# Performance work log

Hardware: AMD Instinct MI355X
Metric: run time of the kernel (lower is better)

## Reference

```python
import jax, jax.numpy as jnp
import numpy as np

RADIUS = 0.2
K = 32  # num_neighbors


def ball_query(centers, points, radius, k):
    """centers [B,3,M], points [B,3,N] -> int32 indices [B,M,k].
    Matches PointNet++ CUDA semantics: first k points (in original order)
    with squared distance < radius^2; slots beyond the count are filled
    with the first valid index (0 if no point is in the ball)."""
    cn = jnp.sum(centers * centers, axis=1)              # [B,M]
    pn = jnp.sum(points * points, axis=1)                # [B,N]
    cross = jnp.einsum('bdm,bdn->bmn', centers, points)  # [B,M,N]
    d2 = cn[:, :, None] + pn[:, None, :] - 2.0 * cross   # [B,M,N]
    valid = d2 < radius * radius
    # stable argsort puts valid indices first, preserving original order
    order = jnp.argsort(jnp.logical_not(valid), axis=-1, stable=True)
    idx = order[..., :k]                                  # [B,M,k]
    count = jnp.sum(valid, axis=-1, keepdims=True)        # [B,M,1]
    fill = idx[..., :1]                                   # first valid (or 0)
    return jnp.where(jnp.arange(k)[None, None, :] < count, idx, fill)


def group(features, idx):
    """features [B,C,N], idx [B,M,K] -> [B,C,M,K]."""
    return jax.vmap(lambda f, i: jnp.take(f, i, axis=1))(features, idx)


def setup_inputs() -> dict:
    key = jax.random.key(0)
    k1, k2, k3, k4 = jax.random.split(key, 4)
    B, N, M, C, CT = 8, 8192, 2048, 64, 64
    return {
        'points_coords': jax.random.uniform(k1, (B, 3, N), dtype=jnp.float32),
        'centers_coords': jax.random.uniform(k2, (B, 3, M), dtype=jnp.float32),
        'temb': jax.random.normal(k3, (B, CT, N), dtype=jnp.float32),
        'points_features': jax.random.normal(k4, (B, C, N), dtype=jnp.float32),
    }


def reference(points_coords, centers_coords, temb, points_features):
    idx = ball_query(centers_coords, points_coords, RADIUS, K)           # [B,M,K]
    neighbor_coords = group(points_coords, idx) - centers_coords[:, :, :, None]  # [B,3,M,K]
    neighbor_features = jnp.concatenate(
        [neighbor_coords, group(points_features, idx)], axis=1)          # [B,3+C,M,K]
    temb_grouped = group(temb, idx)                                      # [B,CT,M,K]
    return neighbor_features, temb_grouped
```

## Files before the change

### kernel.cpp

```cpp
#include <hip/hip_runtime.h>

#define B  8
#define N  8192
#define M  2048
#define C  64
#define CT 64
#define K  32
#define R2 0.04f

__global__ __launch_bounds__(256) void transpose_kernel(
    const float* __restrict__ points,
    const float* __restrict__ temb,
    const float* __restrict__ feats,
    float* __restrict__ pointsT,
    float* __restrict__ tembT,
    float* __restrict__ featsT)
{
    const int gx = blockIdx.x;
    if (gx < 2048) {
        const int a  = gx >> 10;
        const int tt = gx & 1023;
        const int b  = tt >> 7;
        const int n0 = (tt & 127) << 6;
        const float* src = (a ? temb : feats) + (size_t)b * 64 * N;
        float* dst = (a ? tembT : featsT) + (size_t)b * N * 64;
        __shared__ float lds[64][65];
        const int nl = threadIdx.x & 63;
        const int c0 = threadIdx.x >> 6;
        #pragma unroll
        for (int i = 0; i < 16; ++i) {
            const int c = c0 + i * 4;
            lds[c][nl] = src[(size_t)c * N + n0 + nl];
        }
        __syncthreads();
        #pragma unroll
        for (int i = 0; i < 16; ++i) {
            const int n = c0 + i * 4;
            dst[(size_t)(n0 + n) * 64 + nl] = lds[nl][n];
        }
    } else {
        const int tt = gx - 2048;
        const int b  = tt >> 5;
        const int n  = ((tt & 31) << 8) + threadIdx.x;
        const float* pc = points + (size_t)b * 3 * N;
        float* dst = pointsT + ((size_t)b * N + n) * 4;
        dst[0] = pc[n];
        dst[1] = pc[N + n];
        dst[2] = pc[2 * N + n];
    }
}

__global__ __launch_bounds__(256) void ball_query_kernel(
    const float* __restrict__ points,
    const float* __restrict__ centers,
    int* __restrict__ idx)
{
    __shared__ int sidx[4][K];
    const int wave = threadIdx.x >> 6;
    const int lane = threadIdx.x & 63;
    const int center_id = blockIdx.x * 4 + wave;
    const int b = center_id / M;
    const int m = center_id - b * M;

    const float* pc = points + b * 3 * N;
    const float cx = centers[(b * 3 + 0) * M + m];
    const float cy = centers[(b * 3 + 1) * M + m];
    const float cz = centers[(b * 3 + 2) * M + m];
    const float cn = __fadd_rn(__fadd_rn(__fmul_rn(cx, cx), __fmul_rn(cy, cy)),
                               __fmul_rn(cz, cz));

    if (lane == 0) sidx[wave][0] = 0;

    int cnt = 0;
    for (int base = 0; base < N; base += 64) {
        const int n = base + lane;
        const float px = pc[n];
        const float py = pc[N + n];
        const float pz = pc[2 * N + n];
        const float pn = __fadd_rn(__fadd_rn(__fmul_rn(px, px), __fmul_rn(py, py)),
                                   __fmul_rn(pz, pz));
        const float cross = __fadd_rn(__fadd_rn(__fmul_rn(cx, px), __fmul_rn(cy, py)),
                                      __fmul_rn(cz, pz));
        const float d2 = __fsub_rn(__fadd_rn(cn, pn), __fmul_rn(2.0f, cross));
        const bool valid = d2 < R2;
        const unsigned long long mask = __ballot(valid);
        if (valid) {
            const int slot = cnt + __popcll(mask & ((1ull << lane) - 1ull));
            if (slot < K) sidx[wave][slot] = n;
        }
        cnt += (int)__popcll(mask);
        if (cnt >= K) break;
    }
    __syncthreads();

    if (lane < K) {
        const int fill = sidx[wave][0];
        const int v = sidx[wave][lane];
        idx[center_id * K + lane] = (lane < cnt) ? v : fill;
    }
}

__global__ __launch_bounds__(256) void gather_kernel(
    const float* __restrict__ pointsT,
    const float* __restrict__ centers,
    const float* __restrict__ tembT,
    const float* __restrict__ featsT,
    const int* __restrict__ idx,
    float* __restrict__ out1,
    float* __restrict__ out2)
{
    __shared__ int   sn[128];
    __shared__ float tile[128 * 65];
    __shared__ float ctile[3][128];

    const int t = threadIdx.x;
    const int MB4 = M / 4;
    const int b  = blockIdx.x / MB4;
    const int m0 = (blockIdx.x - b * MB4) * 4;
    const size_t base_mk = (size_t)m0 * K;
    const size_t cs = (size_t)M * K;

    if (t < 128) sn[t] = idx[((size_t)b * M + m0) * K + t];
    __syncthreads();

    const int cq = t & 15;
    const int pl = t >> 4;
    const float* fT = featsT + (size_t)b * N * 64;
    const float* tT = tembT  + (size_t)b * N * 64;

    #pragma unroll
    for (int i = 0; i < 8; ++i) {
        const int p = i * 16 + pl;
        const int n = sn[p];
        const float4 v = *(const float4*)(fT + (size_t)n * 64 + cq * 4);
        float* d = &tile[p * 65 + cq * 4];
        d[0] = v.x; d[1] = v.y; d[2] = v.z; d[3] = v.w;
    }
    __syncthreads();
    {
        const int p   = t & 127;
        const int ch0 = t >> 7;
        float* o = out1 + (size_t)b * 67 * cs + 3 * cs + base_mk + p;
        #pragma unroll
        for (int i = 0; i < 32; ++i) {
            const int c = ch0 + i * 2;
            o[(size_t)c * cs] = tile[p * 65 + c];
        }
    }
    __syncthreads();

    #pragma unroll
    for (int i = 0; i < 8; ++i) {
        const int p = i * 16 + pl;
        const int n = sn[p];
        const float4 v = *(const float4*)(tT + (size_t)n * 64 + cq * 4);
        float* d = &tile[p * 65 + cq * 4];
        d[0] = v.x; d[1] = v.y; d[2] = v.z; d[3] = v.w;
    }
    __syncthreads();
    {
        const int p   = t & 127;
        const int ch0 = t >> 7;
        float* o = out2 + (size_t)b * 64 * cs + base_mk + p;
        #pragma unroll
        for (int i = 0; i < 32; ++i) {
            const int c = ch0 + i * 2;
            o[(size_t)c * cs] = tile[p * 65 + c];
        }
    }

    if (t < 128) {
        const int p = t;
        const int n = sn[p];
        const int m = m0 + (p >> 5);
        const float4 v = *(const float4*)(pointsT + ((size_t)b * N + n) * 4);
        ctile[0][p] = v.x - centers[((size_t)b * 3 + 0) * M + m];
        ctile[1][p] = v.y - centers[((size_t)b * 3 + 1) * M + m];
        ctile[2][p] = v.z - centers[((size_t)b * 3 + 2) * M + m];
    }
    __syncthreads();
    {
        const int c = t >> 7;
        const int p = t & 127;
        out1[((size_t)b * 67 + c) * cs + base_mk + p] = ctile[c][p];
    }
    if (t < 128) {
        out1[((size_t)b * 67 + 2) * cs + base_mk + t] = ctile[2][t];
    }
}

extern "C" void kernel_launch(void* const* d_in, const int* in_sizes, int n_in,
                              void* d_out, int out_size, void* d_ws, size_t ws_size,
                              hipStream_t stream) {
    const float* points  = (const float*)d_in[0];
    const float* centers = (const float*)d_in[1];
    const float* temb    = (const float*)d_in[2];
    const float* feats   = (const float*)d_in[3];

    int*   idx     = (int*)d_ws;
    float* pointsT = (float*)((char*)d_ws + (2u << 20));
    float* featsT  = pointsT + (size_t)B * N * 4;
    float* tembT   = featsT  + (size_t)B * N * 64;

    float* out1 = (float*)d_out;
    float* out2 = out1 + (size_t)B * (3 + C) * M * K;

    transpose_kernel<<<2304, 256, 0, stream>>>(points, temb, feats,
                                               pointsT, tembT, featsT);
    ball_query_kernel<<<(B * M) / 4, 256, 0, stream>>>(points, centers, idx);
    gather_kernel<<<(B * M) / 4, 256, 0, stream>>>(pointsT, centers, tembT,
                                                   featsT, idx, out1, out2);
}
```

Before: 382.3 us.

## Fuse ball query into gather kernel with prefetched float4 point loads

Merges the ball-query kernel into the gather kernel. Each wave now finds its center's neighbor indices straight into shared memory, so the idx buffer round trip and one launch go away. The search reads the transposed float4 point array in batches of 8, double-buffered, and uses mbcnt to rank lanes. The cost is more registers in the fused kernel, and the block's gather phase now waits on the slowest wave's search.

```diff
diff --git a/kernel.cpp b/kernel.cpp
--- a/kernel.cpp
+++ b/kernel.cpp
@@ -47,65 +47,37 @@
         dst[0] = pc[n];
         dst[1] = pc[N + n];
         dst[2] = pc[2 * N + n];
+        dst[3] = 0.0f;
     }
 }
 
-__global__ __launch_bounds__(256) void ball_query_kernel(
-    const float* __restrict__ points,
-    const float* __restrict__ centers,
-    int* __restrict__ idx)
-{
-    __shared__ int sidx[4][K];
-    const int wave = threadIdx.x >> 6;
-    const int lane = threadIdx.x & 63;
-    const int center_id = blockIdx.x * 4 + wave;
-    const int b = center_id / M;
-    const int m = center_id - b * M;
-
-    const float* pc = points + b * 3 * N;
-    const float cx = centers[(b * 3 + 0) * M + m];
-    const float cy = centers[(b * 3 + 1) * M + m];
-    const float cz = centers[(b * 3 + 2) * M + m];
-    const float cn = __fadd_rn(__fadd_rn(__fmul_rn(cx, cx), __fmul_rn(cy, cy)),
-                               __fmul_rn(cz, cz));
-
-    if (lane == 0) sidx[wave][0] = 0;
-
-    int cnt = 0;
-    for (int base = 0; base < N; base += 64) {
-        const int n = base + lane;
-        const float px = pc[n];
-        const float py = pc[N + n];
-        const float pz = pc[2 * N + n];
-        const float pn = __fadd_rn(__fadd_rn(__fmul_rn(px, px), __fmul_rn(py, py)),
-                                   __fmul_rn(pz, pz));
-        const float cross = __fadd_rn(__fadd_rn(__fmul_rn(cx, px), __fmul_rn(cy, py)),
-                                      __fmul_rn(cz, pz));
-        const float d2 = __fsub_rn(__fadd_rn(cn, pn), __fmul_rn(2.0f, cross));
-        const bool valid = d2 < R2;
-        const unsigned long long mask = __ballot(valid);
-        if (valid) {
-            const int slot = cnt + __popcll(mask & ((1ull << lane) - 1ull));
-            if (slot < K) sidx[wave][slot] = n;
-        }
-        cnt += (int)__popcll(mask);
-        if (cnt >= K) break;
-    }
-    __syncthreads();
-
-    if (lane < K) {
-        const int fill = sidx[wave][0];
-        const int v = sidx[wave][lane];
-        idx[center_id * K + lane] = (lane < cnt) ? v : fill;
-    }
-}
-
-__global__ __launch_bounds__(256) void gather_kernel(
+#define PROC(vv, nn)                                                          \
+    do {                                                                      \
+        const float px = (vv).x, py = (vv).y, pz = (vv).z;                    \
+        const float pn2 = __fadd_rn(                                          \
+            __fadd_rn(__fmul_rn(px, px), __fmul_rn(py, py)),                  \
+            __fmul_rn(pz, pz));                                               \
+        const float cross = __fadd_rn(                                        \
+            __fadd_rn(__fmul_rn(cx, px), __fmul_rn(cy, py)),                  \
+            __fmul_rn(cz, pz));                                               \
+        const float d2 = __fsub_rn(__fadd_rn(cn, pn2),                        \
+                                   __fmul_rn(2.0f, cross));                   \
+        const bool valid = d2 < R2;                                           \
+        const unsigned long long mask = __ballot(valid);                      \
+        if (valid) {                                                          \
+            const int slot = cnt + __builtin_amdgcn_mbcnt_hi(                 \
+                (unsigned)(mask >> 32),                                       \
+                __builtin_amdgcn_mbcnt_lo((unsigned)mask, 0));                \
+            if (slot < K) sn[wv * K + slot] = (nn);                           \
+        }                                                                     \
+        cnt += (int)__popcll(mask);                                           \
+    } while (0)
+
+__global__ __launch_bounds__(256) void fused_kernel(
     const float* __restrict__ pointsT,
     const float* __restrict__ centers,
     const float* __restrict__ tembT,
     const float* __restrict__ featsT,
-    const int* __restrict__ idx,
     float* __restrict__ out1,
     float* __restrict__ out2)
 {
@@ -120,7 +92,51 @@
     const size_t base_mk = (size_t)m0 * K;
     const size_t cs = (size_t)M * K;
 
-    if (t < 128) sn[t] = idx[((size_t)b * M + m0) * K + t];
+    {
+        const int wv   = t >> 6;
+        const int lane = t & 63;
+        const int m    = m0 + wv;
+        const float cx = centers[((size_t)b * 3 + 0) * M + m];
+        const float cy = centers[((size_t)b * 3 + 1) * M + m];
+        const float cz = centers[((size_t)b * 3 + 2) * M + m];
+        const float cn = __fadd_rn(
+            __fadd_rn(__fmul_rn(cx, cx), __fmul_rn(cy, cy)),
+            __fmul_rn(cz, cz));
+
+        if (lane == 0) sn[wv * K] = 0;
+
+        const float4* pt4 = (const float4*)(pointsT + (size_t)b * N * 4);
+        int cnt = 0;
+        float4 va[8], vb[8];
+        #pragma unroll
+        for (int j = 0; j < 8; ++j) va[j] = pt4[j * 64 + lane];
+
+        for (int g = 0; g < 16; g += 2) {
+            if (g + 1 < 16) {
+                #pragma unroll
+                for (int j = 0; j < 8; ++j)
+                    vb[j] = pt4[((g + 1) * 8 + j) * 64 + lane];
+            }
+            #pragma unroll
+            for (int j = 0; j < 8; ++j) PROC(va[j], g * 512 + j * 64 + lane);
+            if (cnt >= K || g + 1 >= 16) break;
+
+            if (g + 2 < 16) {
+                #pragma unroll
+                for (int j = 0; j < 8; ++j)
+                    va[j] = pt4[((g + 2) * 8 + j) * 64 + lane];
+            }
+            #pragma unroll
+            for (int j = 0; j < 8; ++j) PROC(vb[j], (g + 1) * 512 + j * 64 + lane);
+            if (cnt >= K) break;
+        }
+
+        if (lane < K) {
+            const int fill = sn[wv * K];
+            const int v    = sn[wv * K + lane];
+            sn[wv * K + lane] = (lane < cnt) ? v : fill;
+        }
+    }
     __syncthreads();
 
     const int cq = t & 15;
@@ -197,8 +213,7 @@
     const float* temb    = (const float*)d_in[2];
     const float* feats   = (const float*)d_in[3];
 
-    int*   idx     = (int*)d_ws;
-    float* pointsT = (float*)((char*)d_ws + (2u << 20));
+    float* pointsT = (float*)d_ws;
     float* featsT  = pointsT + (size_t)B * N * 4;
     float* tembT   = featsT  + (size_t)B * N * 64;
 
@@ -207,7 +222,6 @@
 
     transpose_kernel<<<2304, 256, 0, stream>>>(points, temb, feats,
                                                pointsT, tembT, featsT);
-    ball_query_kernel<<<(B * M) / 4, 256, 0, stream>>>(points, centers, idx);
-    gather_kernel<<<(B * M) / 4, 256, 0, stream>>>(pointsT, centers, tembT,
-                                                   featsT, idx, out1, out2);
+    fused_kernel<<<(B * M) / 4, 256, 0, stream>>>(pointsT, centers, tembT,
+                                                  featsT, out1, out2);
 }
```

New measurement: 328.6 us. -14.0%, faster.

## Pipeline ball-query loads from packed float4 points with precomputed norms

Applied to the files above, without the earlier changes.

The transpose kernel now stores each point's squared norm in the fourth slot of the packed pointsT array. The ball query reads these float4s, processing 256 points per step with double-buffered prefetch of the next group. It also uses mbcnt for the lane prefix count and drops the block barrier. This targets load latency and per-point arithmetic in the early-exit scan. The cost is extra registers and possible wasted loads past the break point.

```diff
diff --git a/kernel.cpp b/kernel.cpp
--- a/kernel.cpp
+++ b/kernel.cpp
@@ -44,14 +44,37 @@
         const int n  = ((tt & 31) << 8) + threadIdx.x;
         const float* pc = points + (size_t)b * 3 * N;
         float* dst = pointsT + ((size_t)b * N + n) * 4;
-        dst[0] = pc[n];
-        dst[1] = pc[N + n];
-        dst[2] = pc[2 * N + n];
-    }
-}
+        const float px = pc[n];
+        const float py = pc[N + n];
+        const float pz = pc[2 * N + n];
+        dst[0] = px;
+        dst[1] = py;
+        dst[2] = pz;
+        dst[3] = __fadd_rn(__fadd_rn(__fmul_rn(px, px), __fmul_rn(py, py)),
+                           __fmul_rn(pz, pz));
+    }
+}
+
+#define PROC(vv, nn)                                                          \
+    do {                                                                      \
+        const float cross = __fadd_rn(                                        \
+            __fadd_rn(__fmul_rn(cx, (vv).x), __fmul_rn(cy, (vv).y)),          \
+            __fmul_rn(cz, (vv).z));                                           \
+        const float d2 = __fsub_rn(__fadd_rn(cn, (vv).w),                     \
+                                   __fmul_rn(2.0f, cross));                   \
+        const bool valid = d2 < R2;                                           \
+        const unsigned long long mask = __ballot(valid);                      \
+        if (valid) {                                                          \
+            const int slot = cnt + __builtin_amdgcn_mbcnt_hi(                 \
+                (unsigned)(mask >> 32),                                       \
+                __builtin_amdgcn_mbcnt_lo((unsigned)mask, 0));                \
+            if (slot < K) snp[slot] = (nn);                                   \
+        }                                                                     \
+        cnt += (int)__popcll(mask);                                           \
+    } while (0)
 
 __global__ __launch_bounds__(256) void ball_query_kernel(
-    const float* __restrict__ points,
+    const float* __restrict__ pointsT,
     const float* __restrict__ centers,
     int* __restrict__ idx)
 {
@@ -59,44 +82,48 @@
     const int wave = threadIdx.x >> 6;
     const int lane = threadIdx.x & 63;
     const int center_id = blockIdx.x * 4 + wave;
-    const int b = center_id / M;
-    const int m = center_id - b * M;
-
-    const float* pc = points + b * 3 * N;
-    const float cx = centers[(b * 3 + 0) * M + m];
-    const float cy = centers[(b * 3 + 1) * M + m];
-    const float cz = centers[(b * 3 + 2) * M + m];
+    const int b = center_id >> 11;
+    const int m = center_id & (M - 1);
+
+    const float cx = centers[((size_t)b * 3 + 0) * M + m];
+    const float cy = centers[((size_t)b * 3 + 1) * M + m];
+    const float cz = centers[((size_t)b * 3 + 2) * M + m];
     const float cn = __fadd_rn(__fadd_rn(__fmul_rn(cx, cx), __fmul_rn(cy, cy)),
                                __fmul_rn(cz, cz));
 
-    if (lane == 0) sidx[wave][0] = 0;
-
+    int* snp = sidx[wave];
+    if (lane == 0) snp[0] = 0;
+
+    const float4* pt4 = (const float4*)(pointsT + (size_t)b * N * 4);
     int cnt = 0;
-    for (int base = 0; base < N; base += 64) {
-        const int n = base + lane;
-        const float px = pc[n];
-        const float py = pc[N + n];
-        const float pz = pc[2 * N + n];
-        const float pn = __fadd_rn(__fadd_rn(__fmul_rn(px, px), __fmul_rn(py, py)),
-                                   __fmul_rn(pz, pz));
-        const float cross = __fadd_rn(__fadd_rn(__fmul_rn(cx, px), __fmul_rn(cy, py)),
-                                      __fmul_rn(cz, pz));
-        const float d2 = __fsub_rn(__fadd_rn(cn, pn), __fmul_rn(2.0f, cross));
-        const bool valid = d2 < R2;
-        const unsigned long long mask = __ballot(valid);
-        if (valid) {
-            const int slot = cnt + __popcll(mask & ((1ull << lane) - 1ull));
-            if (slot < K) sidx[wave][slot] = n;
-        }
-        cnt += (int)__popcll(mask);
+    float4 va[4], vb[4];
+    #pragma unroll
+    for (int j = 0; j < 4; ++j) va[j] = pt4[j * 64 + lane];
+
+    for (int g = 0; g < 32; g += 2) {
+        if (g + 1 < 32) {
+            #pragma unroll
+            for (int j = 0; j < 4; ++j)
+                vb[j] = pt4[((g + 1) * 4 + j) * 64 + lane];
+        }
+        #pragma unroll
+        for (int j = 0; j < 4; ++j) PROC(va[j], g * 256 + j * 64 + lane);
+        if (cnt >= K || g + 1 >= 32) break;
+
+        if (g + 2 < 32) {
+            #pragma unroll
+            for (int j = 0; j < 4; ++j)
+                va[j] = pt4[((g + 2) * 4 + j) * 64 + lane];
+        }
+        #pragma unroll
+        for (int j = 0; j < 4; ++j) PROC(vb[j], (g + 1) * 256 + j * 64 + lane);
         if (cnt >= K) break;
     }
-    __syncthreads();
 
     if (lane < K) {
-        const int fill = sidx[wave][0];
-        const int v = sidx[wave][lane];
-        idx[center_id * K + lane] = (lane < cnt) ? v : fill;
+        const int fill = snp[0];
+        const int v    = snp[lane];
+        idx[(size_t)center_id * K + lane] = (lane < cnt) ? v : fill;
     }
 }
 
@@ -207,7 +234,7 @@
 
     transpose_kernel<<<2304, 256, 0, stream>>>(points, temb, feats,
                                                pointsT, tembT, featsT);
-    ball_query_kernel<<<(B * M) / 4, 256, 0, stream>>>(points, centers, idx);
+    ball_query_kernel<<<(B * M) / 4, 256, 0, stream>>>(pointsT, centers, idx);
     gather_kernel<<<(B * M) / 4, 256, 0, stream>>>(pointsT, centers, tembT,
                                                    featsT, idx, out1, out2);
 }
```

After: 334.9 us. 12.4% less time.
